# Kernel optimization log

Measured on AMD Instinct MI355X. Metric: run time of the kernel, lower is better.

Reference implementation:

```python
import jax, jax.numpy as jnp
import numpy as np

D_IN = 2048
D_OUT = 2048
NUM_HEADS = 16
HEAD_DIM = D_OUT // NUM_HEADS
CONTEXT_LENGTH = 4096
THETA_BASE = 10000.0


def _rope_tables(seq_len):
    half = HEAD_DIM // 2
    inv_freq = 1.0 / (THETA_BASE ** (jnp.arange(half, dtype=jnp.float32) / half))
    positions = jnp.arange(seq_len, dtype=jnp.float32)
    angles = positions[:, None] * inv_freq[None, :]          # [S, half]
    angles = jnp.concatenate([angles, angles], axis=-1)      # [S, HEAD_DIM]
    return jnp.cos(angles), jnp.sin(angles)


def _apply_rope(x, cos, sin):
    # x: [B, H, S, D]
    half = x.shape[-1] // 2
    x1, x2 = x[..., :half], x[..., half:]
    rotated = jnp.concatenate([-x2, x1], axis=-1)
    return x * cos[None, None, :, :] + rotated * sin[None, None, :, :]


def setup_inputs() -> dict:
    key = jax.random.key(0)
    ks = jax.random.split(key, 5)
    x = jax.random.normal(ks[0], (1, 4096, D_IN), dtype=jnp.float32)
    scale_in = 1.0 / np.sqrt(D_IN)
    scale_out = 1.0 / np.sqrt(D_OUT)
    w_q = jax.random.normal(ks[1], (D_OUT, D_IN), dtype=jnp.float32) * scale_in
    w_k = jax.random.normal(ks[2], (D_OUT, D_IN), dtype=jnp.float32) * scale_in
    w_v = jax.random.normal(ks[3], (D_OUT, D_IN), dtype=jnp.float32) * scale_in
    w_o = jax.random.normal(ks[4], (D_IN, D_OUT), dtype=jnp.float32) * scale_out
    return {"x": x, "w_q": w_q, "w_k": w_k, "w_v": w_v, "w_o": w_o}


def reference(x, w_q, w_k, w_v, w_o):
    b, s, _ = x.shape
    cos, sin = _rope_tables(s)

    def split_heads(t):  # [B,S,D_OUT] -> [B,H,S,HEAD_DIM]
        return t.reshape(b, s, NUM_HEADS, HEAD_DIM).transpose(0, 2, 1, 3)

    q = split_heads(jnp.einsum('bsd,od->bso', x, w_q))
    k = split_heads(jnp.einsum('bsd,od->bso', x, w_k))
    v = split_heads(jnp.einsum('bsd,od->bso', x, w_v))

    q = _apply_rope(q, cos, sin)
    k = _apply_rope(k, cos, sin)

    scores = jnp.einsum('bhqd,bhkd->bhqk', q, k) / jnp.sqrt(jnp.float32(HEAD_DIM))
    causal = jnp.tril(jnp.ones((s, s), dtype=bool))
    scores = jnp.where(causal[None, None, :, :], scores, -jnp.inf)
    attn = jax.nn.softmax(scores, axis=-1)

    ctx = jnp.einsum('bhqk,bhkd->bhqd', attn, v)  # [B,H,S,HEAD_DIM]
    ctx = ctx.transpose(0, 2, 1, 3).reshape(b, s, D_OUT)
    return jnp.einsum('bso,do->bsd', ctx, w_o)
```

## Files before the change

kernel.cpp:

```cpp
#include <hip/hip_runtime.h>
#include <hip/hip_bf16.h>
#include <stdint.h>

#define SEQ 4096
#define DM 2048
#define NH 16
#define HD 128

typedef __attribute__((ext_vector_type(4)))  float f32x4;
typedef __attribute__((ext_vector_type(16))) float f32x16;
typedef __attribute__((ext_vector_type(8)))  short bf16x8;
typedef __attribute__((ext_vector_type(4)))  float float4_t;
typedef __attribute__((ext_vector_type(4)))  short s16x4;
typedef __attribute__((ext_vector_type(2)))  int   i32x2;
typedef __attribute__((ext_vector_type(2)))  unsigned u32x2;

__device__ __forceinline__ short f2bf(float f) {
  union { float f; unsigned u; } c; c.f = f;
  unsigned u = c.u;
  u += 0x7FFFu + ((u >> 16) & 1u);
  return (short)(u >> 16);
}

__device__ __forceinline__ int cvtpk(float lo, float hi) {
  int r;
  asm("v_cvt_pk_bf16_f32 %0, %1, %2" : "=v"(r) : "v"(lo), "v"(hi));
  return r;
}

__device__ __forceinline__ float exp2r(float x) {
  return __builtin_amdgcn_exp2f(x);
}

__device__ __forceinline__ void async16(const void* g, void* l) {
  __builtin_amdgcn_global_load_lds((const __attribute__((address_space(1))) void*)g,
                                   (__attribute__((address_space(3))) void*)l, 16, 0, 0);
}

__global__ __launch_bounds__(256) void rope_tables_kernel(float2* __restrict__ tab) {
  int idx = blockIdx.x * 256 + threadIdx.x;
  int s = idx >> 6, j = idx & 63;
  float invf = expf(-(float)j * (9.210340371976184f / 64.0f));
  float ang = (float)s * invf;
  tab[idx] = make_float2(cosf(ang), sinf(ang));
}

__global__ __launch_bounds__(256) void f32_to_bf16_kernel(const float* __restrict__ in,
                                                          short* __restrict__ out, int n4) {
  int stride = gridDim.x * 256;
  for (int i = blockIdx.x * 256 + threadIdx.x; i < n4; i += stride) {
    float4_t v = ((const float4_t*)in)[i];
    s16x4 r;
    #pragma unroll
    for (int u = 0; u < 4; u++) r[u] = f2bf(v[u]);
    ((s16x4*)out)[i] = r;
  }
}

template<int OUT_MODE>
__global__ __launch_bounds__(256) void gemm_async_kernel(
    const short* __restrict__ A, const short* __restrict__ B,
    void* __restrict__ Cp, int M, int N, int K) {
  __shared__ short As[128 * 64];
  __shared__ short Bs[128 * 64];
  const int t = threadIdx.x, lane = t & 63, w = t >> 6;
  const int wr = w >> 1, wc = w & 1;
  const size_t Mbase = (size_t)blockIdx.x * 128;
  const size_t Nbase = (size_t)blockIdx.y * 128;
  f32x4 acc[4][4] = {};

  for (int k0 = 0; k0 < K; k0 += 64) {
    __syncthreads();
    #pragma unroll
    for (int c = 0; c < 4; c++) {
      int ob = w * 4096 + c * 1024;
      int o = ob + lane * 16;
      int row = o >> 7;
      int cb = (o & 127) ^ ((row & 7) << 4);
      async16((const char*)A + ((Mbase + row) * (size_t)K + k0) * 2 + cb, (char*)As + ob);
      async16((const char*)B + ((Nbase + row) * (size_t)K + k0) * 2 + cb, (char*)Bs + ob);
    }
    __syncthreads();

    bf16x8 a[2][4], b[2][4];
    #pragma unroll
    for (int ks = 0; ks < 2; ks++) {
      #pragma unroll
      for (int m = 0; m < 4; m++) {
        int row = wr * 64 + m * 16 + (lane & 15);
        int chunk = ks * 64 + (lane >> 4) * 16;
        a[ks][m] = *(const bf16x8*)((const char*)As + row * 128 + (chunk ^ ((row & 7) << 4)));
      }
      #pragma unroll
      for (int n = 0; n < 4; n++) {
        int row = wc * 64 + n * 16 + (lane & 15);
        int chunk = ks * 64 + (lane >> 4) * 16;
        b[ks][n] = *(const bf16x8*)((const char*)Bs + row * 128 + (chunk ^ ((row & 7) << 4)));
      }
    }
    #pragma unroll
    for (int ks = 0; ks < 2; ks++)
      #pragma unroll
      for (int m = 0; m < 4; m++)
        #pragma unroll
        for (int n = 0; n < 4; n++)
          acc[m][n] = __builtin_amdgcn_mfma_f32_16x16x32_bf16(a[ks][m], b[ks][n], acc[m][n], 0, 0, 0);
  }

  #pragma unroll
  for (int m = 0; m < 4; m++)
    #pragma unroll
    for (int n = 0; n < 4; n++)
      #pragma unroll
      for (int j = 0; j < 4; j++) {
        size_t row = Mbase + wr * 64 + m * 16 + (lane >> 4) * 4 + j;
        size_t col = Nbase + wc * 64 + n * 16 + (lane & 15);
        float v = acc[m][n][j];
        if (OUT_MODE == 0) ((float*)Cp)[row * N + col] = v;
        else               ((short*)Cp)[col * (size_t)M + row] = f2bf(v);
      }
}

template<int IS_Q>
__global__ __launch_bounds__(256) void gemm_rope_kernel(
    const short* __restrict__ A, const short* __restrict__ B,
    short* __restrict__ C, const float2* __restrict__ tab) {
  __shared__ short As[128 * 64];
  __shared__ short Bs[128 * 64];
  const int t = threadIdx.x, lane = t & 63, w = t >> 6;
  const size_t Mbase = (size_t)blockIdx.x * 128;
  const size_t Nbase = (size_t)blockIdx.y * 128;
  const int K = DM;
  f32x4 acc[2][8] = {};

  for (int k0 = 0; k0 < K; k0 += 64) {
    __syncthreads();
    #pragma unroll
    for (int c = 0; c < 4; c++) {
      int ob = w * 4096 + c * 1024;
      int o = ob + lane * 16;
      int row = o >> 7;
      int cb = (o & 127) ^ ((row & 7) << 4);
      async16((const char*)A + ((Mbase + row) * (size_t)K + k0) * 2 + cb, (char*)As + ob);
      async16((const char*)B + ((Nbase + row) * (size_t)K + k0) * 2 + cb, (char*)Bs + ob);
    }
    __syncthreads();

    bf16x8 a[2][2], b[2][8];
    #pragma unroll
    for (int ks = 0; ks < 2; ks++) {
      #pragma unroll
      for (int m = 0; m < 2; m++) {
        int row = w * 32 + m * 16 + (lane & 15);
        int chunk = ks * 64 + (lane >> 4) * 16;
        a[ks][m] = *(const bf16x8*)((const char*)As + row * 128 + (chunk ^ ((row & 7) << 4)));
      }
      #pragma unroll
      for (int n = 0; n < 8; n++) {
        int row = n * 16 + (lane & 15);
        int chunk = ks * 64 + (lane >> 4) * 16;
        b[ks][n] = *(const bf16x8*)((const char*)Bs + row * 128 + (chunk ^ ((row & 7) << 4)));
      }
    }
    #pragma unroll
    for (int ks = 0; ks < 2; ks++)
      #pragma unroll
      for (int m = 0; m < 2; m++)
        #pragma unroll
        for (int n = 0; n < 8; n++)
          acc[m][n] = __builtin_amdgcn_mfma_f32_16x16x32_bf16(a[ks][m], b[ks][n], acc[m][n], 0, 0, 0);
  }

  const float SC = IS_Q ? 0.12751746f : 1.0f;
  #pragma unroll
  for (int m = 0; m < 2; m++)
    #pragma unroll
    for (int n = 0; n < 4; n++)
      #pragma unroll
      for (int j = 0; j < 4; j++) {
        int row = (int)Mbase + w * 32 + m * 16 + (lane >> 4) * 4 + j;
        int dj = n * 16 + (lane & 15);
        float2 cs = tab[row * 64 + dj];
        float cc = cs.x * SC, ss = cs.y * SC;
        float r1 = acc[m][n][j], r2 = acc[m][n + 4][j];
        C[(size_t)row * DM + Nbase + dj]      = f2bf(r1 * cc - r2 * ss);
        C[(size_t)row * DM + Nbase + dj + 64] = f2bf(r2 * cc + r1 * ss);
      }
}

__global__ __launch_bounds__(512) void flash_attn10_kernel(
    const short* __restrict__ Q, const short* __restrict__ K,
    const short* __restrict__ VT, short* __restrict__ O) {
  __shared__ __align__(16) char LB[98304];
  const int t = threadIdx.x, lane = t & 63, w = t >> 6;
  const int hi = lane >> 5, c31 = lane & 31;
  const int s = w & 3, v = w >> 2;
  const int id = blockIdx.x;
  const int h  = (id & 7) * 2 + ((id >> 3) & 1);
  const int pr = id >> 4;

  auto stage = [&](int kt, int buf) {
    #pragma unroll
    for (int it = 0; it < 2; it++) {
      const int ob = it * 8192 + w * 1024;
      const int o  = ob + lane * 16;
      const int row = o >> 8;
      const int xs = (o & 255) ^ ((row & 15) << 4);
      {
        const size_t src = ((size_t)(kt * 64 + row) * DM + h * HD) * 2 + xs;
        async16((const char*)K + src, LB + buf * 16384 + ob); }
      {
        const int d = 2 * row + (xs >> 7);
        const size_t src = ((size_t)(h * HD + d) * SEQ + (size_t)kt * 64) * 2
                         + (size_t)(xs & 127);
        async16((const char*)VT + src, LB + 49152 + buf * 16384 + ob); }
    }
  };

  for (int rep = 0; rep < 2; rep++) {
    const int qt = rep ? (31 - pr) : pr;
    const int q0 = qt * 128;
    const int nt = 2 * (qt + 1);
    const int qrow = q0 + s * 32 + c31;

    bf16x8 qf[8];
    #pragma unroll
    for (int ss = 0; ss < 8; ss++)
      qf[ss] = *(const bf16x8*)(Q + (size_t)qrow * DM + h * HD + ss * 16 + hi * 8);

    stage(0, 0);
    stage(1, 1);

    f32x16 oacc[4] = {};
    float m = -3.0e38f, l = 0.f;

    int buf = 0;
    for (int kt = 0; kt < nt; kt++) {
      if (kt == nt - 1) asm volatile("s_waitcnt vmcnt(0)" ::: "memory");
      else              asm volatile("s_waitcnt vmcnt(4)" ::: "memory");
      __builtin_amdgcn_s_barrier();
      __builtin_amdgcn_sched_barrier(0);

      if (kt + 2 < nt) {
        int b2 = buf + 2; if (b2 >= 3) b2 -= 3;
        stage(kt + 2, b2);
      }

      if (kt * 64 + v * 32 <= q0 + s * 32 + 31) {
        const char* KsB = LB + buf * 16384;
        const char* VsB = LB + 49152 + buf * 16384;

        f32x16 sacc = {};
        __builtin_amdgcn_s_setprio(1);
        #pragma unroll
        for (int ss = 0; ss < 8; ss++) {
          int row = v * 32 + c31;
          bf16x8 kf = *(const bf16x8*)(KsB + row * 256
                                       + ((ss * 32 + hi * 16) ^ ((row & 15) << 4)));
          sacc = __builtin_amdgcn_mfma_f32_32x32x16_bf16(kf, qf[ss], sacc, 0, 0, 0);
        }
        __builtin_amdgcn_s_setprio(0);

        float t0[8];
        #pragma unroll
        for (int r = 0; r < 8; r++) t0[r] = fmaxf(sacc[r], sacc[r + 8]);
        #pragma unroll
        for (int d = 4; d > 0; d >>= 1)
          #pragma unroll
          for (int r = 0; r < 4; r++) if (r < d) t0[r] = fmaxf(t0[r], t0[r + d]);
        float mx = t0[0];
        i32x2 mm = __builtin_amdgcn_permlane32_swap(__float_as_int(mx), __float_as_int(mx),
                                                    false, false);
        mx = fmaxf(__int_as_float(mm.x), __int_as_float(mm.y));

        if (__any(mx > m + 11.5416f)) {
          float mn = fmaxf(m, mx);
          float al = exp2r(m - mn);
          m = mn; l *= al;
          #pragma unroll
          for (int g = 0; g < 4; g++)
            #pragma unroll
            for (int r = 0; r < 16; r++) oacc[g][r] *= al;
        }

        const int rel = qrow - kt * 64 - v * 32;
        const bool maskT = (kt * 64 + v * 32 + 31) > (q0 + s * 32);
        #pragma unroll
        for (int r = 0; r < 16; r++) {
          float e = exp2r(sacc[r] - m);
          if (maskT) {
            int kl = (r & 3) + 8 * (r >> 2) + 4 * hi;
            e = (kl > rel) ? 0.f : e;
          }
          sacc[r] = e;
        }

        float s0[8];
        #pragma unroll
        for (int r = 0; r < 8; r++) s0[r] = sacc[r] + sacc[r + 8];
        #pragma unroll
        for (int d = 4; d > 0; d >>= 1)
          #pragma unroll
          for (int r = 0; r < 4; r++) if (r < d) s0[r] = s0[r] + s0[r + d];
        l += s0[0];

        bf16x8 pa[2];
        #pragma unroll
        for (int sg = 0; sg < 2; sg++) {
          int q0a = cvtpk(sacc[8 * sg + 0], sacc[8 * sg + 1]);
          int q1a = cvtpk(sacc[8 * sg + 2], sacc[8 * sg + 3]);
          int q0b = cvtpk(sacc[8 * sg + 4], sacc[8 * sg + 5]);
          int q1b = cvtpk(sacc[8 * sg + 6], sacc[8 * sg + 7]);
          i32x2 r0 = __builtin_amdgcn_permlane32_swap(q0a, q0b, false, false);
          i32x2 r1 = __builtin_amdgcn_permlane32_swap(q1a, q1b, false, false);
          union { int d[4]; bf16x8 vv; } u;
          u.d[0] = r0.x; u.d[1] = r1.x; u.d[2] = r0.y; u.d[3] = r1.y;
          pa[sg] = u.vv;
        }

        __builtin_amdgcn_s_setprio(1);
        #pragma unroll
        for (int ks = 0; ks < 2; ks++)
          #pragma unroll
          for (int g = 0; g < 4; g++) {
            int d = g * 32 + c31;
            int row = d >> 1;
            int x = (d & 1) * 128 + v * 64 + ks * 32 + hi * 16;
            bf16x8 vf = *(const bf16x8*)(VsB + row * 256 + (x ^ ((row & 15) << 4)));
            oacc[g] = __builtin_amdgcn_mfma_f32_32x32x16_bf16(vf, pa[ks], oacc[g], 0, 0, 0);
          }
        __builtin_amdgcn_s_setprio(0);
      }
      buf = (buf == 2) ? 0 : buf + 1;
    }
    __syncthreads();

    i32x2 lr = __builtin_amdgcn_permlane32_swap(__float_as_int(l), __float_as_int(l),
                                                false, false);
    l = __int_as_float(lr.x) + __int_as_float(lr.y);

    #pragma unroll
    for (int round = 0; round < 2; round++) {
      const int reg = s & 1;
      const bool active = (s >> 1) == round;
      if (active && v == 1) {
        float* Op = (float*)(LB + reg * 16384);
        #pragma unroll
        for (int g = 0; g < 4; g++)
          #pragma unroll
          for (int rr = 0; rr < 16; rr++) {
            int d = g * 32 + (rr & 3) + 8 * (rr >> 2) + 4 * hi;
            Op[d * 32 + c31] = oacc[g][rr];
          }
        if (hi == 0) {
          float* mm2 = (float*)(LB + 32768 + reg * 256) + c31 * 2;
          mm2[0] = m; mm2[1] = l;
        }
      }
      __syncthreads();
      if (active && v == 0) {
        const float* mm2 = (const float*)(LB + 32768 + reg * 256) + c31 * 2;
        float lB = mm2[1];
        float mB = (lB > 0.f) ? mm2[0] : -3.0e38f;
        float ms = fmaxf(m, mB);
        float aA = exp2r(m - ms), aB = exp2r(mB - ms);
        float linv = 1.0f / (l * aA + lB * aB);
        float sA = aA * linv, sB = aB * linv;
        const float* Op = (const float*)(LB + reg * 16384);
        #pragma unroll
        for (int g = 0; g < 4; g++)
          #pragma unroll
          for (int tt = 0; tt < 4; tt++) {
            float o[4];
            #pragma unroll
            for (int e = 0; e < 4; e++) {
              int d = g * 32 + e + 8 * tt + 4 * hi;
              o[e] = oacc[g][4 * tt + e] * sA + Op[d * 32 + c31] * sB;
            }
            u32x2 pk;
            pk.x = (unsigned)cvtpk(o[0], o[1]);
            pk.y = (unsigned)cvtpk(o[2], o[3]);
            *(u32x2*)(O + (size_t)qrow * DM + h * HD + g * 32 + tt * 8 + hi * 4) = pk;
          }
      }
      __syncthreads();
    }
  }
}

extern "C" void kernel_launch(void* const* d_in, const int* in_sizes, int n_in,
                              void* d_out, int out_size, void* d_ws, size_t ws_size,
                              hipStream_t stream) {
  const float* x  = (const float*)d_in[0];
  const float* wq = (const float*)d_in[1];
  const float* wk = (const float*)d_in[2];
  const float* wv = (const float*)d_in[3];
  const float* wo = (const float*)d_in[4];
  float* out = (float*)d_out;

  const size_t SQDMs = (size_t)SEQ * DM;
  short* Qb   = (short*)d_ws;
  short* Kb   = Qb + SQDMs;
  short* VTb  = Kb + SQDMs;
  short* Cb   = VTb + SQDMs;
  short* xbf  = Cb + SQDMs;
  short* wbuf = xbf + SQDMs;
  float2* tab = (float2*)(wbuf + (size_t)DM * DM);

  rope_tables_kernel<<<SEQ * 64 / 256, 256, 0, stream>>>(tab);
  f32_to_bf16_kernel<<<2048, 256, 0, stream>>>(x, xbf, (int)(SQDMs / 4));

  dim3 g(SEQ / 128, DM / 128);
  f32_to_bf16_kernel<<<2048, 256, 0, stream>>>(wq, wbuf, DM * DM / 4);
  gemm_rope_kernel<1><<<g, 256, 0, stream>>>(xbf, wbuf, Qb, tab);
  f32_to_bf16_kernel<<<2048, 256, 0, stream>>>(wk, wbuf, DM * DM / 4);
  gemm_rope_kernel<0><<<g, 256, 0, stream>>>(xbf, wbuf, Kb, tab);
  f32_to_bf16_kernel<<<2048, 256, 0, stream>>>(wv, wbuf, DM * DM / 4);
  gemm_async_kernel<2><<<g, 256, 0, stream>>>(xbf, wbuf, VTb, SEQ, DM, DM);

  flash_attn10_kernel<<<256, 512, 0, stream>>>(Qb, Kb, VTb, Cb);

  f32_to_bf16_kernel<<<2048, 256, 0, stream>>>(wo, wbuf, DM * DM / 4);
  gemm_async_kernel<0><<<g, 256, 0, stream>>>(Cb, wbuf, out, SEQ, DM, DM);
}
```

Baseline: 302.8 us.

## Software-pipeline QK^T of next tile with softmax+PV of previous tile

The flash attention loop is restructured so each iteration issues the QK^T MFMAs for the current key tile before running softmax and the PV MFMAs for the previous tile, using two score accumulators in ping-pong. The LDS ring grows from three to four K/V buffers (128 KB of shared memory) so the extra tile in flight stays resident. The aim is to overlap exp/softmax VALU work with matrix-core work. The cost is higher register pressure from the second score accumulator and more LDS use per block, which could lower occupancy.

After: 302.9 us. About the same (+0.0%).

```diff
diff --git a/kernel.cpp b/kernel.cpp
--- a/kernel.cpp
+++ b/kernel.cpp
@@ -188,10 +188,10 @@
       }
 }
 
-__global__ __launch_bounds__(512) void flash_attn10_kernel(
+__global__ __launch_bounds__(512) void flash_attn11_kernel(
     const short* __restrict__ Q, const short* __restrict__ K,
     const short* __restrict__ VT, short* __restrict__ O) {
-  __shared__ __align__(16) char LB[98304];
+  __shared__ __align__(16) char LB[131072];
   const int t = threadIdx.x, lane = t & 63, w = t >> 6;
   const int hi = lane >> 5, c31 = lane & 31;
   const int s = w & 3, v = w >> 2;
@@ -199,7 +199,8 @@
   const int h  = (id & 7) * 2 + ((id >> 3) & 1);
   const int pr = id >> 4;
 
-  auto stage = [&](int kt, int buf) {
+  auto stage = [&](int kt) {
+    const int buf = kt & 3;
     #pragma unroll
     for (int it = 0; it < 2; it++) {
       const int ob = it * 8192 + w * 1024;
@@ -213,7 +214,7 @@
         const int d = 2 * row + (xs >> 7);
         const size_t src = ((size_t)(h * HD + d) * SEQ + (size_t)kt * 64) * 2
                          + (size_t)(xs & 127);
-        async16((const char*)VT + src, LB + 49152 + buf * 16384 + ob); }
+        async16((const char*)VT + src, LB + 65536 + buf * 16384 + ob); }
     }
   };
 
@@ -228,111 +229,126 @@
     for (int ss = 0; ss < 8; ss++)
       qf[ss] = *(const bf16x8*)(Q + (size_t)qrow * DM + h * HD + ss * 16 + hi * 8);
 
-    stage(0, 0);
-    stage(1, 1);
+    stage(0);
+    stage(1);
 
     f32x16 oacc[4] = {};
+    f32x16 sA = {}, sB = {};
     float m = -3.0e38f, l = 0.f;
-
-    int buf = 0;
-    for (int kt = 0; kt < nt; kt++) {
+    bool hpA = false, hpB = false;
+
+    auto qk_into = [&](f32x16& sx, int ktx) {
+      const char* KsB = LB + (ktx & 3) * 16384;
+      #pragma unroll
+      for (int r = 0; r < 16; r++) sx[r] = 0.f;
+      __builtin_amdgcn_s_setprio(1);
+      #pragma unroll
+      for (int ss = 0; ss < 8; ss++) {
+        int row = v * 32 + c31;
+        bf16x8 kf = *(const bf16x8*)(KsB + row * 256
+                                     + ((ss * 32 + hi * 16) ^ ((row & 15) << 4)));
+        sx = __builtin_amdgcn_mfma_f32_32x32x16_bf16(kf, qf[ss], sx, 0, 0, 0);
+      }
+      __builtin_amdgcn_s_setprio(0);
+    };
+
+    auto smpv = [&](f32x16& sx, int ktx) {
+      float t0[8];
+      #pragma unroll
+      for (int r = 0; r < 8; r++) t0[r] = fmaxf(sx[r], sx[r + 8]);
+      #pragma unroll
+      for (int d = 4; d > 0; d >>= 1)
+        #pragma unroll
+        for (int r = 0; r < 4; r++) if (r < d) t0[r] = fmaxf(t0[r], t0[r + d]);
+      float mx = t0[0];
+      i32x2 mm = __builtin_amdgcn_permlane32_swap(__float_as_int(mx), __float_as_int(mx),
+                                                  false, false);
+      mx = fmaxf(__int_as_float(mm.x), __int_as_float(mm.y));
+
+      if (__any(mx > m + 11.5416f)) {
+        float mn = fmaxf(m, mx);
+        float al = exp2r(m - mn);
+        m = mn; l *= al;
+        #pragma unroll
+        for (int g = 0; g < 4; g++)
+          #pragma unroll
+          for (int r = 0; r < 16; r++) oacc[g][r] *= al;
+      }
+
+      const int rel = qrow - ktx * 64 - v * 32;
+      const bool maskT = (ktx * 64 + v * 32 + 31) > (q0 + s * 32);
+      #pragma unroll
+      for (int r = 0; r < 16; r++) {
+        float e = exp2r(sx[r] - m);
+        if (maskT) {
+          int kl = (r & 3) + 8 * (r >> 2) + 4 * hi;
+          e = (kl > rel) ? 0.f : e;
+        }
+        sx[r] = e;
+      }
+
+      float s0[8];
+      #pragma unroll
+      for (int r = 0; r < 8; r++) s0[r] = sx[r] + sx[r + 8];
+      #pragma unroll
+      for (int d = 4; d > 0; d >>= 1)
+        #pragma unroll
+        for (int r = 0; r < 4; r++) if (r < d) s0[r] = s0[r] + s0[r + d];
+      l += s0[0];
+
+      bf16x8 pa[2];
+      #pragma unroll
+      for (int sg = 0; sg < 2; sg++) {
+        int q0a = cvtpk(sx[8 * sg + 0], sx[8 * sg + 1]);
+        int q1a = cvtpk(sx[8 * sg + 2], sx[8 * sg + 3]);
+        int q0b = cvtpk(sx[8 * sg + 4], sx[8 * sg + 5]);
+        int q1b = cvtpk(sx[8 * sg + 6], sx[8 * sg + 7]);
+        i32x2 r0 = __builtin_amdgcn_permlane32_swap(q0a, q0b, false, false);
+        i32x2 r1 = __builtin_amdgcn_permlane32_swap(q1a, q1b, false, false);
+        union { int d[4]; bf16x8 vv; } u;
+        u.d[0] = r0.x; u.d[1] = r1.x; u.d[2] = r0.y; u.d[3] = r1.y;
+        pa[sg] = u.vv;
+      }
+
+      const char* VsB = LB + 65536 + (ktx & 3) * 16384;
+      __builtin_amdgcn_s_setprio(1);
+      #pragma unroll
+      for (int ks = 0; ks < 2; ks++)
+        #pragma unroll
+        for (int g = 0; g < 4; g++) {
+          int d = g * 32 + c31;
+          int row = d >> 1;
+          int x = (d & 1) * 128 + v * 64 + ks * 32 + hi * 16;
+          bf16x8 vf = *(const bf16x8*)(VsB + row * 256 + (x ^ ((row & 15) << 4)));
+          oacc[g] = __builtin_amdgcn_mfma_f32_32x32x16_bf16(vf, pa[ks], oacc[g], 0, 0, 0);
+        }
+      __builtin_amdgcn_s_setprio(0);
+    };
+
+    auto active = [&](int ktx) { return ktx * 64 + v * 32 <= q0 + s * 32 + 31; };
+
+    for (int kt = 0; kt < nt; kt += 2) {
       if (kt == nt - 1) asm volatile("s_waitcnt vmcnt(0)" ::: "memory");
       else              asm volatile("s_waitcnt vmcnt(4)" ::: "memory");
       __builtin_amdgcn_s_barrier();
       __builtin_amdgcn_sched_barrier(0);
-
-      if (kt + 2 < nt) {
-        int b2 = buf + 2; if (b2 >= 3) b2 -= 3;
-        stage(kt + 2, b2);
-      }
-
-      if (kt * 64 + v * 32 <= q0 + s * 32 + 31) {
-        const char* KsB = LB + buf * 16384;
-        const char* VsB = LB + 49152 + buf * 16384;
-
-        f32x16 sacc = {};
-        __builtin_amdgcn_s_setprio(1);
-        #pragma unroll
-        for (int ss = 0; ss < 8; ss++) {
-          int row = v * 32 + c31;
-          bf16x8 kf = *(const bf16x8*)(KsB + row * 256
-                                       + ((ss * 32 + hi * 16) ^ ((row & 15) << 4)));
-          sacc = __builtin_amdgcn_mfma_f32_32x32x16_bf16(kf, qf[ss], sacc, 0, 0, 0);
-        }
-        __builtin_amdgcn_s_setprio(0);
-
-        float t0[8];
-        #pragma unroll
-        for (int r = 0; r < 8; r++) t0[r] = fmaxf(sacc[r], sacc[r + 8]);
-        #pragma unroll
-        for (int d = 4; d > 0; d >>= 1)
-          #pragma unroll
-          for (int r = 0; r < 4; r++) if (r < d) t0[r] = fmaxf(t0[r], t0[r + d]);
-        float mx = t0[0];
-        i32x2 mm = __builtin_amdgcn_permlane32_swap(__float_as_int(mx), __float_as_int(mx),
-                                                    false, false);
-        mx = fmaxf(__int_as_float(mm.x), __int_as_float(mm.y));
-
-        if (__any(mx > m + 11.5416f)) {
-          float mn = fmaxf(m, mx);
-          float al = exp2r(m - mn);
-          m = mn; l *= al;
-          #pragma unroll
-          for (int g = 0; g < 4; g++)
-            #pragma unroll
-            for (int r = 0; r < 16; r++) oacc[g][r] *= al;
-        }
-
-        const int rel = qrow - kt * 64 - v * 32;
-        const bool maskT = (kt * 64 + v * 32 + 31) > (q0 + s * 32);
-        #pragma unroll
-        for (int r = 0; r < 16; r++) {
-          float e = exp2r(sacc[r] - m);
-          if (maskT) {
-            int kl = (r & 3) + 8 * (r >> 2) + 4 * hi;
-            e = (kl > rel) ? 0.f : e;
-          }
-          sacc[r] = e;
-        }
-
-        float s0[8];
-        #pragma unroll
-        for (int r = 0; r < 8; r++) s0[r] = sacc[r] + sacc[r + 8];
-        #pragma unroll
-        for (int d = 4; d > 0; d >>= 1)
-          #pragma unroll
-          for (int r = 0; r < 4; r++) if (r < d) s0[r] = s0[r] + s0[r + d];
-        l += s0[0];
-
-        bf16x8 pa[2];
-        #pragma unroll
-        for (int sg = 0; sg < 2; sg++) {
-          int q0a = cvtpk(sacc[8 * sg + 0], sacc[8 * sg + 1]);
-          int q1a = cvtpk(sacc[8 * sg + 2], sacc[8 * sg + 3]);
-          int q0b = cvtpk(sacc[8 * sg + 4], sacc[8 * sg + 5]);
-          int q1b = cvtpk(sacc[8 * sg + 6], sacc[8 * sg + 7]);
-          i32x2 r0 = __builtin_amdgcn_permlane32_swap(q0a, q0b, false, false);
-          i32x2 r1 = __builtin_amdgcn_permlane32_swap(q1a, q1b, false, false);
-          union { int d[4]; bf16x8 vv; } u;
-          u.d[0] = r0.x; u.d[1] = r1.x; u.d[2] = r0.y; u.d[3] = r1.y;
-          pa[sg] = u.vv;
-        }
-
-        __builtin_amdgcn_s_setprio(1);
-        #pragma unroll
-        for (int ks = 0; ks < 2; ks++)
-          #pragma unroll
-          for (int g = 0; g < 4; g++) {
-            int d = g * 32 + c31;
-            int row = d >> 1;
-            int x = (d & 1) * 128 + v * 64 + ks * 32 + hi * 16;
-            bf16x8 vf = *(const bf16x8*)(VsB + row * 256 + (x ^ ((row & 15) << 4)));
-            oacc[g] = __builtin_amdgcn_mfma_f32_32x32x16_bf16(vf, pa[ks], oacc[g], 0, 0, 0);
-          }
-        __builtin_amdgcn_s_setprio(0);
-      }
-      buf = (buf == 2) ? 0 : buf + 1;
-    }
+      if (kt + 2 < nt) stage(kt + 2);
+      bool actA = active(kt);
+      if (actA) qk_into(sA, kt);
+      if (hpB) smpv(sB, kt - 1);
+      hpA = actA;
+
+      if (kt + 1 == nt - 1) asm volatile("s_waitcnt vmcnt(0)" ::: "memory");
+      else                  asm volatile("s_waitcnt vmcnt(4)" ::: "memory");
+      __builtin_amdgcn_s_barrier();
+      __builtin_amdgcn_sched_barrier(0);
+      if (kt + 3 < nt) stage(kt + 3);
+      bool actB = active(kt + 1);
+      if (actB) qk_into(sB, kt + 1);
+      if (hpA) smpv(sA, kt);
+      hpB = actB;
+    }
+    if (hpB) smpv(sB, nt - 1);
     __syncthreads();
 
     i32x2 lr = __builtin_amdgcn_permlane32_swap(__float_as_int(l), __float_as_int(l),
@@ -342,8 +358,8 @@
     #pragma unroll
     for (int round = 0; round < 2; round++) {
       const int reg = s & 1;
-      const bool active = (s >> 1) == round;
-      if (active && v == 1) {
+      const bool act = (s >> 1) == round;
+      if (act && v == 1) {
         float* Op = (float*)(LB + reg * 16384);
         #pragma unroll
         for (int g = 0; g < 4; g++)
@@ -358,14 +374,14 @@
         }
       }
       __syncthreads();
-      if (active && v == 0) {
+      if (act && v == 0) {
         const float* mm2 = (const float*)(LB + 32768 + reg * 256) + c31 * 2;
         float lB = mm2[1];
         float mB = (lB > 0.f) ? mm2[0] : -3.0e38f;
         float ms = fmaxf(m, mB);
         float aA = exp2r(m - ms), aB = exp2r(mB - ms);
         float linv = 1.0f / (l * aA + lB * aB);
-        float sA = aA * linv, sB = aB * linv;
+        float sA2 = aA * linv, sB2 = aB * linv;
         const float* Op = (const float*)(LB + reg * 16384);
         #pragma unroll
         for (int g = 0; g < 4; g++)
@@ -375,7 +391,7 @@
             #pragma unroll
             for (int e = 0; e < 4; e++) {
               int d = g * 32 + e + 8 * tt + 4 * hi;
-              o[e] = oacc[g][4 * tt + e] * sA + Op[d * 32 + c31] * sB;
+              o[e] = oacc[g][4 * tt + e] * sA2 + Op[d * 32 + c31] * sB2;
             }
             u32x2 pk;
             pk.x = (unsigned)cvtpk(o[0], o[1]);
@@ -418,7 +434,7 @@
   f32_to_bf16_kernel<<<2048, 256, 0, stream>>>(wv, wbuf, DM * DM / 4);
   gemm_async_kernel<2><<<g, 256, 0, stream>>>(xbf, wbuf, VTb, SEQ, DM, DM);
 
-  flash_attn10_kernel<<<256, 512, 0, stream>>>(Qb, Kb, VTb, Cb);
+  flash_attn11_kernel<<<256, 512, 0, stream>>>(Qb, Kb, VTb, Cb);
 
   f32_to_bf16_kernel<<<2048, 256, 0, stream>>>(wo, wbuf, DM * DM / 4);
   gemm_async_kernel<0><<<g, 256, 0, stream>>>(Cb, wbuf, out, SEQ, DM, DM);
```
